# Performance work log

Measured on AMD Instinct MI355X. Metric: run time of the kernel, lower is better.

Reference implementation:

```python
import jax, jax.numpy as jnp
import numpy as np

B, P, ENC, DEC, ATT, EMB, V, MEM, TCAP = 64, 196, 2048, 512, 512, 512, 10000, 128, 22
T = TCAP - 1  # max decode length (caption_lengths - 1)


def setup_inputs() -> dict:
    key = jax.random.key(0)
    ks = iter(jax.random.split(key, 32))
    def w(shape, s=0.02):
        return (jax.random.normal(next(ks), shape, jnp.float32) * s)
    encoder_out = jax.random.normal(next(ks), (B, P, ENC), jnp.float32)
    encoded_captions = jax.random.randint(next(ks), (B, TCAP), 0, V)
    lens = np.sort(np.asarray(jax.random.randint(next(ks), (B,), 5, TCAP + 1)))[::-1].copy()
    lens[0] = TCAP  # ensure max(decode_lengths) == T
    caption_lengths = jnp.asarray(lens, jnp.int32)
    return {
        'encoder_out': encoder_out,
        'encoded_captions': encoded_captions,
        'caption_lengths': caption_lengths,
        'emb_table': w((V, EMB), 0.05),
        # Linear weights stored as [in, out] (torch W.T), so y = x @ W + b
        'W_enc': w((ENC, ATT)), 'b_enc': jnp.zeros((ATT,), jnp.float32),
        'W_dec': w((DEC, ATT)), 'b_dec': jnp.zeros((ATT,), jnp.float32),
        'W_full': w((ATT, 1)), 'b_full': jnp.zeros((1,), jnp.float32),
        'W_inith': w((ENC, DEC)), 'b_inith': jnp.zeros((DEC,), jnp.float32),
        'W_initc': w((ENC, DEC)), 'b_initc': jnp.zeros((DEC,), jnp.float32),
        'W_beta': w((DEC, ENC)), 'b_beta': jnp.zeros((ENC,), jnp.float32),
        # LSTMCell (torch gate order i, f, g, o), stored as [in, 4*dec]
        'W_ih': w((EMB + ENC, 4 * DEC)), 'b_ih': jnp.zeros((4 * DEC,), jnp.float32),
        'W_hh': w((DEC, 4 * DEC)), 'b_hh': jnp.zeros((4 * DEC,), jnp.float32),
        'memory_bank': jax.random.normal(next(ks), (MEM, DEC), jnp.float32),
        'W_fc': w((DEC, V)), 'b_fc': jnp.zeros((V,), jnp.float32),
    }


def _decode(encoder_out, encoded_captions, caption_lengths, emb_table,
            W_enc, b_enc, W_dec, b_dec, W_full, b_full,
            W_inith, b_inith, W_initc, b_initc, W_beta, b_beta,
            W_ih, b_ih, W_hh, b_hh, memory_bank, W_fc, b_fc):
    dec_len = caption_lengths - 1  # decode_lengths
    embs = emb_table[encoded_captions]                 # [B, TCAP, EMB]
    mean_enc = encoder_out.mean(axis=1)                # [B, ENC]
    h0 = mean_enc @ W_inith + b_inith
    c0 = mean_enc @ W_initc + b_initc
    att1 = encoder_out @ W_enc + b_enc                 # [B, P, ATT] precomputed

    x_seq = jnp.swapaxes(embs[:, :T, :], 0, 1)         # [T, B, EMB]
    mask_seq = jnp.arange(T)[:, None] < dec_len[None, :]  # [T, B]

    def step(carry, inp):
        h, c = carry
        x_t, m = inp                                   # [B,EMB], [B]
        # attention
        att2 = h @ W_dec + b_dec                       # [B, ATT]
        e = (jax.nn.relu(att1 + att2[:, None, :]) @ W_full)[..., 0] + b_full[0]  # [B, P]
        alpha = jax.nn.softmax(e, axis=1)
        awe = jnp.einsum('bpe,bp->be', encoder_out, alpha)  # [B, ENC]
        gate = jax.nn.sigmoid(h @ W_beta + b_beta)
        awe = gate * awe
        # LSTMCell
        xi = jnp.concatenate([x_t, awe], axis=1)
        gates = xi @ W_ih + b_ih + h @ W_hh + b_hh      # [B, 4*DEC]
        gi, gf, gg, go = jnp.split(gates, 4, axis=1)
        c_new = jax.nn.sigmoid(gf) * c + jax.nn.sigmoid(gi) * jnp.tanh(gg)
        h_new = jax.nn.sigmoid(go) * jnp.tanh(c_new)
        # hash memory
        sim = h_new @ memory_bank.T                    # [B, MEM]
        h_new = h_new + jax.nn.softmax(sim, axis=1) @ memory_bank
        # fc (dropout = identity in eval)
        preds = h_new @ W_fc + b_fc                    # [B, V]
        m2 = m[:, None]
        h = jnp.where(m2, h_new, h)
        c = jnp.where(m2, c_new, c)
        preds = jnp.where(m2, preds, 0.0)
        alpha = jnp.where(m2, alpha, 0.0)
        return (h, c), (preds, alpha)

    (_, _), (preds_seq, alpha_seq) = jax.lax.scan(step, (h0, c0), (x_seq, mask_seq))
    predictions = jnp.swapaxes(preds_seq, 0, 1)        # [B, T, V]
    alphas = jnp.swapaxes(alpha_seq, 0, 1)             # [B, T, P]
    return predictions, dec_len, alphas


def reference(encoder_out, encoded_captions, caption_lengths, emb_table,
              W_enc, b_enc, W_dec, b_dec, W_full, b_full,
              W_inith, b_inith, W_initc, b_initc, W_beta, b_beta,
              W_ih, b_ih, W_hh, b_hh, memory_bank, W_fc, b_fc):
    return _decode(encoder_out, encoded_captions, caption_lengths, emb_table,
                   W_enc, b_enc, W_dec, b_dec, W_full, b_full,
                   W_inith, b_inith, W_initc, b_initc, W_beta, b_beta,
                   W_ih, b_ih, W_hh, b_hh, memory_bank, W_fc, b_fc)
```

## Files before the change

### kernel.cpp

```cpp
#include <hip/hip_runtime.h>

#define BB   64
#define PP   196
#define ENCD 2048
#define DECD 512
#define VV   10000
#define TT   21
#define KIH  2560

typedef __attribute__((ext_vector_type(8))) short bf16x8;
typedef __attribute__((ext_vector_type(4))) float f32x4;

__device__ __forceinline__ float sigm(float x)   { return 1.f / (1.f + __expf(-x)); }
__device__ __forceinline__ float tanh_f(float x) { return 1.f - 2.f / (1.f + __expf(2.f * x)); }
__device__ __forceinline__ ushort f2bf(float x) {
    unsigned u = __float_as_uint(x);
    unsigned r = (u + 0x7FFFu + ((u >> 16) & 1u)) >> 16;
    return (ushort)r;
}
__device__ __forceinline__ float bf2f(short u) {
    return __uint_as_float(((unsigned)(ushort)u) << 16);
}
union U8 { float4 f4; ushort u[8]; };


__global__ void k_cvt(const float* __restrict__ in, ushort* __restrict__ out, int n4) {
    int i = blockIdx.x * 256 + threadIdx.x;
    if (i >= n4) return;
    float4 v = ((const float4*)in)[i];
    ushort4 o; o.x = f2bf(v.x); o.y = f2bf(v.y); o.z = f2bf(v.z); o.w = f2bf(v.w);
    ((ushort4*)out)[i] = o;
}

__global__ void k_mean16(const ushort* __restrict__ encB, float* __restrict__ mean) {
    int idx = blockIdx.x * 256 + threadIdx.x;
    int b = idx >> 10, e2 = idx & 1023;
    const uint* p = (const uint*)encB + (size_t)b * PP * 1024 + e2;
    float s0 = 0.f, s1 = 0.f;
    #pragma unroll 7
    for (int i = 0; i < PP; ++i) {
        uint v = p[(size_t)i * 1024];
        s0 += __uint_as_float(v << 16);
        s1 += __uint_as_float(v & 0xffff0000u);
    }
    mean[b * 2048 + e2 * 2]     = s0 * (1.f / 196.f);
    mean[b * 2048 + e2 * 2 + 1] = s1 * (1.f / 196.f);
}

__global__ __launch_bounds__(256) void k_ipart(const float* __restrict__ mean,
        const float* __restrict__ Wh, const float* __restrict__ Wc,
        float* __restrict__ ipart) {
    __shared__ alignas(16) float As[32][68];
    __shared__ alignas(16) float Bs[32][68];
    const int n0 = blockIdx.x * 64;
    const int kc = blockIdx.y;
    const int mat = blockIdx.z;
    const float* Bp = mat ? Wc : Wh;
    const int tid = threadIdx.x, tx = tid & 15, ty = tid >> 4;
    float acc[4][4] = {};
    for (int k0 = 0; k0 < 512; k0 += 32) {
        #pragma unroll
        for (int p = 0; p < 2; ++p) {
            int c = p * 256 + tid;
            int m = c >> 3, k4 = (c & 7) * 4;
            float4 v = *(const float4*)(mean + m * 2048 + kc * 512 + k0 + k4);
            As[k4 + 0][m] = v.x; As[k4 + 1][m] = v.y; As[k4 + 2][m] = v.z; As[k4 + 3][m] = v.w;
            int kb = c >> 4, n4 = (c & 15) * 4;
            float4 w = *(const float4*)(Bp + (size_t)(kc * 512 + k0 + kb) * 512 + n0 + n4);
            *(float4*)&Bs[kb][n4] = w;
        }
        __syncthreads();
        #pragma unroll 8
        for (int k = 0; k < 32; ++k) {
            float4 a = *(const float4*)&As[k][ty * 4];
            float4 b = *(const float4*)&Bs[k][tx * 4];
            float av[4] = {a.x, a.y, a.z, a.w}, bv[4] = {b.x, b.y, b.z, b.w};
            #pragma unroll
            for (int i = 0; i < 4; ++i)
                #pragma unroll
                for (int j = 0; j < 4; ++j) acc[i][j] += av[i] * bv[j];
        }
        __syncthreads();
    }
    #pragma unroll
    for (int i = 0; i < 4; ++i) {
        int m = ty * 4 + i;
        #pragma unroll
        for (int j = 0; j < 4; ++j) {
            int n = n0 + tx * 4 + j;
            ipart[((size_t)(mat * 4 + kc) * BB + m) * 512 + n] = acc[i][j];
        }
    }
}

__global__ void k_ifin(const float* __restrict__ ipart,
                       const float* __restrict__ bh, const float* __restrict__ bc,
                       float* __restrict__ h, float* __restrict__ c, ushort* __restrict__ hB) {
    int idx = blockIdx.x * 256 + threadIdx.x;
    int mat = idx >> 15, rem = idx & 32767;
    int b = rem >> 9, d = rem & 511;
    float s = 0.f;
    #pragma unroll
    for (int kc = 0; kc < 4; ++kc) s += ipart[((size_t)(mat * 4 + kc) * BB + b) * 512 + d];
    if (mat) c[rem] = s + bc[d];
    else { float v = s + bh[d]; h[rem] = v; hB[rem] = f2bf(v); }
}

__global__ __launch_bounds__(256) void k_tcvt_all(
        const float* __restrict__ Wenc, const float* __restrict__ Wdec,
        const float* __restrict__ Wbeta, const float* __restrict__ Whh,
        const float* __restrict__ Wih, const float* __restrict__ Wfc,
        ushort* __restrict__ WencT, ushort* __restrict__ WdecT,
        ushort* __restrict__ WbetaT, ushort* __restrict__ WhhT,
        ushort* __restrict__ WihT, ushort* __restrict__ WfcT) {
    __shared__ float lds[64 * 65];
    int l = blockIdx.x;
    const float* in; ushort* out; int K, N, KT;
    if (l < 256)       { in = Wenc;  out = WencT;  K = 2048; N = 512;   KT = 32; }
    else if (l < 320)  { l -= 256;  in = Wdec;  out = WdecT;  K = 512;  N = 512;   KT = 8; }
    else if (l < 576)  { l -= 320;  in = Wbeta; out = WbetaT; K = 512;  N = 2048;  KT = 8; }
    else if (l < 832)  { l -= 576;  in = Whh;   out = WhhT;   K = 512;  N = 2048;  KT = 8; }
    else if (l < 2112) { l -= 832;  in = Wih;   out = WihT;   K = KIH;  N = 2048;  KT = 40; }
    else               { l -= 2112; in = Wfc;   out = WfcT;   K = 512;  N = 10000; KT = 8; }
    const int k0 = (l % KT) * 64, n0 = (l / KT) * 64;
    const int tid = threadIdx.x;
    for (int i = tid; i < 4096; i += 256) {
        int kk = i >> 6, nn = i & 63;
        float v = 0.f;
        if (n0 + nn < N) v = in[(size_t)(k0 + kk) * N + n0 + nn];
        lds[nn * 65 + kk] = v;
    }
    __syncthreads();
    for (int i = tid; i < 4096; i += 256) {
        int nn = i >> 6, kk = i & 63;
        out[(size_t)(n0 + nn) * K + k0 + kk] = f2bf(lds[nn * 65 + kk]);
    }
}

__global__ __launch_bounds__(256) void k_att1_256(const ushort* __restrict__ A,
        const ushort* __restrict__ Bt, const float* __restrict__ bias,
        ushort* __restrict__ C) {
    __shared__ alignas(16) ushort As[64 * 64];
    __shared__ alignas(16) ushort Bs[256 * 64];
    const int n0 = blockIdx.x * 256;
    const int m0 = blockIdx.y * 64;
    const int tid = threadIdx.x, wid = tid >> 6, lane = tid & 63;
    f32x4 acc[4][4] = {};
    for (int k0 = 0; k0 < 2048; k0 += 64) {
        #pragma unroll
        for (int p = 0; p < 2; ++p) {
            int c = p * 256 + tid;
            int r = c >> 3, cc = c & 7;
            float4 v = *(const float4*)(A + (size_t)(m0 + r) * 2048 + k0 + cc * 8);
            *(float4*)(As + r * 64 + ((cc ^ (r & 7)) * 8)) = v;
        }
        #pragma unroll
        for (int p = 0; p < 8; ++p) {
            int c = p * 256 + tid;
            int r = c >> 3, cc = c & 7;
            float4 v = *(const float4*)(Bt + (size_t)(n0 + r) * 2048 + k0 + cc * 8);
            *(float4*)(Bs + r * 64 + ((cc ^ (r & 7)) * 8)) = v;
        }
        __syncthreads();
        #pragma unroll
        for (int kk = 0; kk < 2; ++kk) {
            int ci = kk * 4 + (lane >> 4);
            bf16x8 afrag[4], bfrag[4];
            #pragma unroll
            for (int m = 0; m < 4; ++m) {
                int row = m * 16 + (lane & 15);
                afrag[m] = *(const bf16x8*)(As + row * 64 + ((ci ^ (row & 7)) * 8));
            }
            #pragma unroll
            for (int n = 0; n < 4; ++n) {
                int col = wid * 64 + n * 16 + (lane & 15);
                bfrag[n] = *(const bf16x8*)(Bs + col * 64 + ((ci ^ (col & 7)) * 8));
            }
            #pragma unroll
            for (int m = 0; m < 4; ++m)
                #pragma unroll
                for (int n = 0; n < 4; ++n)
                    acc[m][n] = __builtin_amdgcn_mfma_f32_16x16x32_bf16(afrag[m], bfrag[n], acc[m][n], 0, 0, 0);
        }
        __syncthreads();
    }
    #pragma unroll
    for (int m = 0; m < 4; ++m) {
        int rb = m0 + m * 16 + (lane >> 4) * 4;
        #pragma unroll
        for (int n = 0; n < 4; ++n) {
            int col = n0 + wid * 64 + n * 16 + (lane & 15);
            float bv = bias[col];
            #pragma unroll
            for (int r = 0; r < 4; ++r)
                C[(size_t)(rb + r) * 512 + col] = f2bf(acc[m][n][r] + bv);
        }
    }
}

__global__ void k_declen(const int* __restrict__ lens, float* __restrict__ out) {
    int b = threadIdx.x;
    if (b < BB) out[b] = (float)(lens[b] - 1);
}


__global__ __launch_bounds__(256) void k_hgemm64(const ushort* __restrict__ hB,
        const float* __restrict__ emb, const int* __restrict__ caps, int t,
        const ushort* __restrict__ WdecT, const float* __restrict__ bd,
        const ushort* __restrict__ WbetaT, const float* __restrict__ bb,
        const ushort* __restrict__ WhhT, const ushort* __restrict__ WihT,
        float* __restrict__ att2, float* __restrict__ gate, float* __restrict__ hhp) {
    __shared__ alignas(16) ushort As[64 * 64];
    __shared__ alignas(16) ushort Bs[64 * 64];
    __shared__ int capsh[64];
    const int bx = blockIdx.x;
    int seg, n0;
    if (bx < 8)       { seg = 0; n0 = bx * 64; }
    else if (bx < 40) { seg = 1; n0 = (bx - 8) * 64; }
    else              { seg = 2; n0 = (bx - 40) * 64; }
    const int tid = threadIdx.x, wid = tid >> 6, lane = tid & 63;
    if (tid < 64) capsh[tid] = caps[tid * 22 + t];
    __syncthreads();
    const int KSEG = (seg == 2) ? 1024 : 512;
    f32x4 acc[4] = {};
    for (int k0 = 0; k0 < KSEG; k0 += 64) {
        const bool second = k0 >= 512;
        #pragma unroll
        for (int p = 0; p < 2; ++p) {
            int c = p * 256 + tid;
            int r = c >> 3, cc = c & 7;
            if (!second) {
                float4 v = *(const float4*)(hB + r * 512 + k0 + cc * 8);
                *(float4*)(As + r * 64 + ((cc ^ (r & 7)) * 8)) = v;
            } else {
                const float* er = emb + (size_t)capsh[r] * 512 + (k0 - 512) + cc * 8;
                float4 v0 = *(const float4*)er;
                float4 v1 = *(const float4*)(er + 4);
                U8 pk;
                pk.u[0] = f2bf(v0.x); pk.u[1] = f2bf(v0.y); pk.u[2] = f2bf(v0.z); pk.u[3] = f2bf(v0.w);
                pk.u[4] = f2bf(v1.x); pk.u[5] = f2bf(v1.y); pk.u[6] = f2bf(v1.z); pk.u[7] = f2bf(v1.w);
                *(float4*)(As + r * 64 + ((cc ^ (r & 7)) * 8)) = pk.f4;
            }
            const ushort* brow;
            if (seg == 0)      brow = WdecT + (size_t)(n0 + r) * 512 + k0 + cc * 8;
            else if (seg == 1) brow = WbetaT + (size_t)(n0 + r) * 512 + k0 + cc * 8;
            else brow = second ? (WihT + (size_t)(n0 + r) * KIH + (k0 - 512) + cc * 8)
                               : (WhhT + (size_t)(n0 + r) * 512 + k0 + cc * 8);
            float4 v = *(const float4*)brow;
            *(float4*)(Bs + r * 64 + ((cc ^ (r & 7)) * 8)) = v;
        }
        __syncthreads();
        #pragma unroll
        for (int kk = 0; kk < 2; ++kk) {
            int ci = kk * 4 + (lane >> 4);
            int colL = wid * 16 + (lane & 15);
            bf16x8 bfrag = *(const bf16x8*)(Bs + colL * 64 + ((ci ^ (colL & 7)) * 8));
            #pragma unroll
            for (int m = 0; m < 4; ++m) {
                int row = m * 16 + (lane & 15);
                bf16x8 afrag = *(const bf16x8*)(As + row * 64 + ((ci ^ (row & 7)) * 8));
                acc[m] = __builtin_amdgcn_mfma_f32_16x16x32_bf16(afrag, bfrag, acc[m], 0, 0, 0);
            }
        }
        __syncthreads();
    }
    int colL = wid * 16 + (lane & 15);
    int col = n0 + colL;
    #pragma unroll
    for (int m = 0; m < 4; ++m) {
        int rb = m * 16 + (lane >> 4) * 4;
        #pragma unroll
        for (int r = 0; r < 4; ++r) {
            int row = rb + r;
            float v = acc[m][r];
            if (seg == 0)      att2[row * 512 + col] = v + bd[col];
            else if (seg == 1) gate[row * 2048 + col] = sigm(v + bb[col]);
            else               hhp[(size_t)row * 2048 + col] = v;
        }
    }
}

__global__ __launch_bounds__(256) void k_escore_p(const ushort* __restrict__ att1B,
        const float* __restrict__ att2, const float* __restrict__ Wf,
        float* __restrict__ es) {
    __shared__ float a2[512], wf[512];
    int b = blockIdx.y, pc = blockIdx.x, tid = threadIdx.x;
    for (int i = tid; i < 512; i += 256) { a2[i] = att2[b * 512 + i]; wf[i] = Wf[i]; }
    __syncthreads();
    int lane = tid & 63, wid = tid >> 6;
    for (int i = wid; i < 49; i += 4) {
        int p = pc * 49 + i;
        bf16x8 rv = *(const bf16x8*)(att1B + ((size_t)(b * PP + p)) * 512 + lane * 8);
        float s = 0.f;
        #pragma unroll
        for (int j = 0; j < 8; ++j) {
            float v = bf2f(rv[j]) + a2[lane * 8 + j];
            s += (v > 0.f ? v : 0.f) * wf[lane * 8 + j];
        }
        #pragma unroll
        for (int off = 32; off; off >>= 1) s += __shfl_down(s, off);
        if (lane == 0) es[b * 256 + p] = s;
    }
}

__global__ __launch_bounds__(256) void k_awe16s(const ushort* __restrict__ encB,
        const float* __restrict__ es, const float* __restrict__ gate,
        const int* __restrict__ lens, int t,
        uint* __restrict__ aweB, float* __restrict__ out_alpha) {
    __shared__ float al[224], red[256];
    int b = blockIdx.y, pc = blockIdx.x, tid = threadIdx.x;
    float v = (tid < PP) ? es[b * 256 + tid] : -3.4e38f;
    red[tid] = v; __syncthreads();
    for (int s = 128; s; s >>= 1) { if (tid < s) red[tid] = fmaxf(red[tid], red[tid + s]); __syncthreads(); }
    float mx = red[0]; __syncthreads();
    float ev = (tid < PP) ? __expf(v - mx) : 0.f;
    red[tid] = ev; __syncthreads();
    for (int s = 128; s; s >>= 1) { if (tid < s) red[tid] += red[tid + s]; __syncthreads(); }
    float inv = 1.f / red[0];
    if (tid < PP) {
        float a = ev * inv;
        al[tid] = a;
        if (pc == 0) {
            bool m = t < (lens[b] - 1);
            out_alpha[((size_t)b * TT + t) * PP + tid] = m ? a : 0.f;
        }
    }
    __syncthreads();
    int pair = pc * 128 + (tid >> 1);
    int half = tid & 1;
    const uint* p = (const uint*)encB + (size_t)b * PP * 1024 + pair;
    float s0 = 0.f, s1 = 0.f;
    int i0 = half * 98;
    #pragma unroll 7
    for (int i = i0; i < i0 + 98; ++i) {
        uint vv = p[(size_t)i * 1024];
        float a = al[i];
        s0 += a * __uint_as_float(vv << 16);
        s1 += a * __uint_as_float(vv & 0xffff0000u);
    }
    s0 += __shfl_xor(s0, 1);
    s1 += __shfl_xor(s1, 1);
    if (half == 0) {
        int e = pair * 2;
        float g0 = s0 * gate[b * 2048 + e];
        float g1 = s1 * gate[b * 2048 + e + 1];
        aweB[b * 1024 + pair] = (uint)f2bf(g0) | ((uint)f2bf(g1) << 16);
    }
}

__global__ __launch_bounds__(256) void k_gawe64(const ushort* __restrict__ aweB,
        const ushort* __restrict__ WihT, float* __restrict__ pawe) {
    __shared__ alignas(16) ushort As[64 * 64];
    __shared__ alignas(16) ushort Bs[64 * 64];
    const int n0 = blockIdx.x * 64;
    const int kc = blockIdx.y;
    const int tid = threadIdx.x, wid = tid >> 6, lane = tid & 63;
    f32x4 acc[4] = {};
    for (int k0 = 0; k0 < 512; k0 += 64) {
        #pragma unroll
        for (int p = 0; p < 2; ++p) {
            int c = p * 256 + tid;
            int r = c >> 3, cc = c & 7;
            float4 v = *(const float4*)(aweB + r * 2048 + kc * 512 + k0 + cc * 8);
            *(float4*)(As + r * 64 + ((cc ^ (r & 7)) * 8)) = v;
            float4 w = *(const float4*)(WihT + (size_t)(n0 + r) * KIH + 512 + kc * 512 + k0 + cc * 8);
            *(float4*)(Bs + r * 64 + ((cc ^ (r & 7)) * 8)) = w;
        }
        __syncthreads();
        #pragma unroll
        for (int kk = 0; kk < 2; ++kk) {
            int ci = kk * 4 + (lane >> 4);
            int colL = wid * 16 + (lane & 15);
            bf16x8 bfrag = *(const bf16x8*)(Bs + colL * 64 + ((ci ^ (colL & 7)) * 8));
            #pragma unroll
            for (int m = 0; m < 4; ++m) {
                int row = m * 16 + (lane & 15);
                bf16x8 afrag = *(const bf16x8*)(As + row * 64 + ((ci ^ (row & 7)) * 8));
                acc[m] = __builtin_amdgcn_mfma_f32_16x16x32_bf16(afrag, bfrag, acc[m], 0, 0, 0);
            }
        }
        __syncthreads();
    }
    int col = n0 + wid * 16 + (lane & 15);
    #pragma unroll
    for (int m = 0; m < 4; ++m) {
        int rb = m * 16 + (lane >> 4) * 4;
        #pragma unroll
        for (int r = 0; r < 4; ++r)
            pawe[((size_t)kc * BB + rb + r) * 2048 + col] = acc[m][r];
    }
}

__global__ __launch_bounds__(256) void k_memattn(const float* __restrict__ hhp,
        const float* __restrict__ pawe,
        const float* __restrict__ bih, const float* __restrict__ bhh,
        const int* __restrict__ lens, int t, const float* __restrict__ memB,
        float* __restrict__ h, float* __restrict__ c,
        ushort* __restrict__ hB, ushort* __restrict__ histB) {
    __shared__ float hs[512], sims[128], red[256], ps[128];
    int b = blockIdx.x, tid = threadIdx.x;
    bool msk = t < (lens[b] - 1);
    for (int j = tid; j < 512; j += 256) {
        float g[4];
        #pragma unroll
        for (int q = 0; q < 4; ++q) {
            int col = q * 512 + j;
            float s = bih[col] + bhh[col] + hhp[(size_t)b * 2048 + col];
            #pragma unroll
            for (int kc = 0; kc < 4; ++kc) s += pawe[((size_t)kc * BB + b) * 2048 + col];
            g[q] = s;
        }
        float gi = sigm(g[0]), gf = sigm(g[1]), gg = tanh_f(g[2]), go = sigm(g[3]);
        float cold = c[b * 512 + j];
        float cn = gf * cold + gi * gg;
        c[b * 512 + j] = msk ? cn : cold;
        hs[j] = go * tanh_f(cn);
    }
    __syncthreads();
    int lane = tid & 63, wid = tid >> 6;
    for (int m = wid * 32; m < wid * 32 + 32; ++m) {
        const float* r = memB + (size_t)m * 512 + lane * 8;
        float4 r0 = *(const float4*)(r);
        float4 r1 = *(const float4*)(r + 4);
        float4 h0 = *(const float4*)(&hs[lane * 8]);
        float4 h1 = *(const float4*)(&hs[lane * 8 + 4]);
        float s = r0.x * h0.x + r0.y * h0.y + r0.z * h0.z + r0.w * h0.w
                + r1.x * h1.x + r1.y * h1.y + r1.z * h1.z + r1.w * h1.w;
        #pragma unroll
        for (int off = 32; off; off >>= 1) s += __shfl_down(s, off);
        if (lane == 0) sims[m] = s;
    }
    __syncthreads();
    float v = (tid < 128) ? sims[tid] : -3.4e38f;
    red[tid] = v; __syncthreads();
    for (int s = 128; s; s >>= 1) { if (tid < s) red[tid] = fmaxf(red[tid], red[tid + s]); __syncthreads(); }
    float mx = red[0]; __syncthreads();
    float ev = (tid < 128) ? __expf(v - mx) : 0.f;
    red[tid] = ev; __syncthreads();
    for (int s = 128; s; s >>= 1) { if (tid < s) red[tid] += red[tid + s]; __syncthreads(); }
    if (tid < 128) ps[tid] = ev / red[0];
    __syncthreads();
    for (int d = tid; d < 512; d += 256) {
        float s = 0.f;
        #pragma unroll 4
        for (int m = 0; m < 128; ++m) s += ps[m] * memB[(size_t)m * 512 + d];
        float hn = hs[d] + s;
        histB[((size_t)t * BB + b) * 512 + d] = f2bf(hn);
        float hold = h[b * 512 + d];
        float hv = msk ? hn : hold;
        h[b * 512 + d] = hv;
        hB[b * 512 + d] = f2bf(hv);
    }
}

__global__ __launch_bounds__(256) void k_preds_batch(const ushort* __restrict__ histB,
        const ushort* __restrict__ WfcT, const float* __restrict__ bfc,
        const int* __restrict__ lens, float* __restrict__ out) {
    __shared__ alignas(16) ushort As[64 * 64];
    __shared__ alignas(16) ushort Bs[256 * 64];
    const int n0 = blockIdx.x * 256;
    const int t = blockIdx.y;
    const ushort* A = histB + (size_t)t * BB * 512;
    const int tid = threadIdx.x, wid = tid >> 6, lane = tid & 63;
    f32x4 acc[4][4] = {};
    for (int k0 = 0; k0 < 512; k0 += 64) {
        #pragma unroll
        for (int p = 0; p < 2; ++p) {
            int c = p * 256 + tid;
            int r = c >> 3, cc = c & 7;
            float4 v = *(const float4*)(A + r * 512 + k0 + cc * 8);
            *(float4*)(As + r * 64 + ((cc ^ (r & 7)) * 8)) = v;
        }
        #pragma unroll
        for (int p = 0; p < 8; ++p) {
            int c = p * 256 + tid;
            int r = c >> 3, cc = c & 7;
            float4 v = *(const float4*)(WfcT + (size_t)(n0 + r) * 512 + k0 + cc * 8);
            *(float4*)(Bs + r * 64 + ((cc ^ (r & 7)) * 8)) = v;
        }
        __syncthreads();
        #pragma unroll
        for (int kk = 0; kk < 2; ++kk) {
            int ci = kk * 4 + (lane >> 4);
            bf16x8 afrag[4], bfrag[4];
            #pragma unroll
            for (int m = 0; m < 4; ++m) {
                int row = m * 16 + (lane & 15);
                afrag[m] = *(const bf16x8*)(As + row * 64 + ((ci ^ (row & 7)) * 8));
            }
            #pragma unroll
            for (int n = 0; n < 4; ++n) {
                int col = wid * 64 + n * 16 + (lane & 15);
                bfrag[n] = *(const bf16x8*)(Bs + col * 64 + ((ci ^ (col & 7)) * 8));
            }
            #pragma unroll
            for (int m = 0; m < 4; ++m)
                #pragma unroll
                for (int n = 0; n < 4; ++n)
                    acc[m][n] = __builtin_amdgcn_mfma_f32_16x16x32_bf16(afrag[m], bfrag[n], acc[m][n], 0, 0, 0);
        }
        __syncthreads();
    }
    #pragma unroll
    for (int m = 0; m < 4; ++m) {
        int rb = m * 16 + (lane >> 4) * 4;
        #pragma unroll
        for (int n = 0; n < 4; ++n) {
            int col = n0 + wid * 64 + n * 16 + (lane & 15);
            if (col < VV) {
                float bv = bfc[col];
                #pragma unroll
                for (int r = 0; r < 4; ++r) {
                    int b = rb + r;
                    bool msk = t < (lens[b] - 1);
                    out[((size_t)b * TT + t) * VV + col] = msk ? (acc[m][n][r] + bv) : 0.f;
                }
            }
        }
    }
}


extern "C" void kernel_launch(void* const* d_in, const int* in_sizes, int n_in,
                              void* d_out, int out_size, void* d_ws, size_t ws_size,
                              hipStream_t stream) {
    const float* enc     = (const float*)d_in[0];
    const int*   caps    = (const int*)d_in[1];
    const int*   lens    = (const int*)d_in[2];
    const float* emb     = (const float*)d_in[3];
    const float* W_enc   = (const float*)d_in[4];
    const float* b_enc   = (const float*)d_in[5];
    const float* W_dec   = (const float*)d_in[6];
    const float* b_dec   = (const float*)d_in[7];
    const float* W_full  = (const float*)d_in[8];
    const float* W_inith = (const float*)d_in[10];
    const float* b_inith = (const float*)d_in[11];
    const float* W_initc = (const float*)d_in[12];
    const float* b_initc = (const float*)d_in[13];
    const float* W_beta  = (const float*)d_in[14];
    const float* b_beta  = (const float*)d_in[15];
    const float* W_ih    = (const float*)d_in[16];
    const float* b_ih    = (const float*)d_in[17];
    const float* W_hh    = (const float*)d_in[18];
    const float* b_hh    = (const float*)d_in[19];
    const float* memB    = (const float*)d_in[20];
    const float* W_fc    = (const float*)d_in[21];
    const float* b_fc    = (const float*)d_in[22];

    float* out = (float*)d_out;
    float* preds_out  = out;
    float* declen_out = out + (size_t)BB * TT * VV;
    float* alpha_out  = declen_out + BB;

    float* ws    = (float*)d_ws;
    ushort* att1B = (ushort*)ws;        ws += (size_t)12544 * 512 / 2;
    float* h     = ws;  ws += BB * DECD;
    float* c     = ws;  ws += BB * DECD;
    float* att2  = ws;  ws += BB * 512;
    float* gate  = ws;  ws += BB * ENCD;
    float* es    = ws;  ws += BB * 256;
    float* hhp   = ws;  ws += BB * 2048;
    float* pawe  = ws;  ws += (size_t)4 * BB * 2048;
    ushort* hB   = (ushort*)ws;  ws += BB * DECD / 2;
    uint*  aweB  = (uint*)ws;    ws += BB * ENCD / 2;
    ushort* histB = (ushort*)ws; ws += (size_t)TT * BB * DECD / 2;
    ushort* encB  = (ushort*)ws; ws += (size_t)12544 * 2048 / 2;
    ushort* WencT = (ushort*)ws; ws += (size_t)512 * 2048 / 2;
    ushort* WfcT  = (ushort*)ws; ws += (size_t)10240 * 512 / 2;
    ushort* WdecT = (ushort*)ws; ws += (size_t)512 * 512 / 2;
    ushort* WbetaT= (ushort*)ws; ws += (size_t)2048 * 512 / 2;
    ushort* WhhT  = (ushort*)ws; ws += (size_t)2048 * 512 / 2;
    ushort* WihT  = (ushort*)ws; ws += (size_t)2048 * KIH / 2;
    float* ipart = hhp;
    float* mean  = (float*)att1B;

    k_cvt<<<(12544 * 2048 / 4 + 255) / 256, 256, 0, stream>>>(enc, encB, 12544 * 2048 / 4);
    k_mean16<<<256, 256, 0, stream>>>(encB, mean);
    k_ipart<<<dim3(8, 4, 2), 256, 0, stream>>>(mean, W_inith, W_initc, ipart);
    k_ifin<<<256, 256, 0, stream>>>(ipart, b_inith, b_initc, h, c, hB);
    k_declen<<<1, 64, 0, stream>>>(lens, declen_out);
    k_tcvt_all<<<3392, 256, 0, stream>>>(W_enc, W_dec, W_beta, W_hh, W_ih, W_fc,
                                         WencT, WdecT, WbetaT, WhhT, WihT, WfcT);
    k_att1_256<<<dim3(2, 196), 256, 0, stream>>>(encB, WencT, b_enc, att1B);

    for (int t = 0; t < TT; ++t) {
        k_hgemm64<<<72, 256, 0, stream>>>(hB, emb, caps, t, WdecT, b_dec, WbetaT, b_beta,
                                          WhhT, WihT, att2, gate, hhp);
        k_escore_p<<<dim3(4, 64), 256, 0, stream>>>(att1B, att2, W_full, es);
        k_awe16s<<<dim3(8, 64), 256, 0, stream>>>(encB, es, gate, lens, t, aweB, alpha_out);
        k_gawe64<<<dim3(32, 4), 256, 0, stream>>>((const ushort*)aweB, WihT, pawe);
        k_memattn<<<64, 256, 0, stream>>>(hhp, pawe, b_ih, b_hh, lens, t, memB, h, c, hB, histB);
    }
    k_preds_batch<<<dim3(40, TT), 256, 0, stream>>>(histB, WfcT, b_fc, lens, preds_out);
}
```

Before: 1.965 ms.

## Precompute embedding input projection for all timesteps and merge recurrent weights

The embedding half of the LSTM input GEMM does not depend on the recurrence, so it is hoisted out of the time loop into one batched GEMM over all timesteps (k_xpre) whose result is read in the gate kernel. The per-step hidden GEMM now uses a single concatenated transposed weight (Wdec|Wbeta|Whh) with uniform K=512, which removes the longer K=1024 segment and the branchy per-segment loads. The attention-weighted encoding kernel is re-split to 16 column chunks with 4 waves striding over pixels plus an LDS reduction. The cost is extra workspace for the per-step precomputed projections.

```diff
diff --git a/kernel.cpp b/kernel.cpp
--- a/kernel.cpp
+++ b/kernel.cpp
@@ -18,8 +18,8 @@
     unsigned r = (u + 0x7FFFu + ((u >> 16) & 1u)) >> 16;
     return (ushort)r;
 }
-__device__ __forceinline__ float bf2f(short u) {
-    return __uint_as_float(((unsigned)(ushort)u) << 16);
+__device__ __forceinline__ float bf2f(ushort u) {
+    return __uint_as_float(((unsigned)u) << 16);
 }
 union U8 { float4 f4; ushort u[8]; };
 
@@ -137,7 +137,7 @@
     }
 }
 
-__global__ __launch_bounds__(256) void k_att1_256(const ushort* __restrict__ A,
+__global__ __launch_bounds__(256) void k_att1n(const ushort* __restrict__ A,
         const ushort* __restrict__ Bt, const float* __restrict__ bias,
         ushort* __restrict__ C) {
     __shared__ alignas(16) ushort As[64 * 64];
@@ -198,56 +198,98 @@
     }
 }
 
+__global__ __launch_bounds__(256) void k_xpre(const float* __restrict__ emb,
+        const int* __restrict__ caps, const ushort* __restrict__ WihT,
+        float* __restrict__ xpre) {
+    __shared__ alignas(16) ushort As[64 * 64];
+    __shared__ alignas(16) ushort Bs[256 * 64];
+    __shared__ int capsh[64];
+    const int n0 = blockIdx.x * 256;
+    const int t = blockIdx.y;
+    const int tid = threadIdx.x, wid = tid >> 6, lane = tid & 63;
+    if (tid < 64) capsh[tid] = caps[tid * 22 + t];
+    __syncthreads();
+    f32x4 acc[4][4] = {};
+    for (int k0 = 0; k0 < 512; k0 += 64) {
+        #pragma unroll
+        for (int p = 0; p < 2; ++p) {
+            int c = p * 256 + tid;
+            int r = c >> 3, cc = c & 7;
+            const float* er = emb + (size_t)capsh[r] * 512 + k0 + cc * 8;
+            float4 v0 = *(const float4*)er;
+            float4 v1 = *(const float4*)(er + 4);
+            U8 pk;
+            pk.u[0] = f2bf(v0.x); pk.u[1] = f2bf(v0.y); pk.u[2] = f2bf(v0.z); pk.u[3] = f2bf(v0.w);
+            pk.u[4] = f2bf(v1.x); pk.u[5] = f2bf(v1.y); pk.u[6] = f2bf(v1.z); pk.u[7] = f2bf(v1.w);
+            *(float4*)(As + r * 64 + ((cc ^ (r & 7)) * 8)) = pk.f4;
+        }
+        #pragma unroll
+        for (int p = 0; p < 8; ++p) {
+            int c = p * 256 + tid;
+            int r = c >> 3, cc = c & 7;
+            float4 v = *(const float4*)(WihT + (size_t)(n0 + r) * KIH + k0 + cc * 8);
+            *(float4*)(Bs + r * 64 + ((cc ^ (r & 7)) * 8)) = v;
+        }
+        __syncthreads();
+        #pragma unroll
+        for (int kk = 0; kk < 2; ++kk) {
+            int ci = kk * 4 + (lane >> 4);
+            bf16x8 afrag[4], bfrag[4];
+            #pragma unroll
+            for (int m = 0; m < 4; ++m) {
+                int row = m * 16 + (lane & 15);
+                afrag[m] = *(const bf16x8*)(As + row * 64 + ((ci ^ (row & 7)) * 8));
+            }
+            #pragma unroll
+            for (int n = 0; n < 4; ++n) {
+                int col = wid * 64 + n * 16 + (lane & 15);
+                bfrag[n] = *(const bf16x8*)(Bs + col * 64 + ((ci ^ (col & 7)) * 8));
+            }
+            #pragma unroll
+            for (int m = 0; m < 4; ++m)
+                #pragma unroll
+                for (int n = 0; n < 4; ++n)
+                    acc[m][n] = __builtin_amdgcn_mfma_f32_16x16x32_bf16(afrag[m], bfrag[n], acc[m][n], 0, 0, 0);
+        }
+        __syncthreads();
+    }
+    #pragma unroll
+    for (int m = 0; m < 4; ++m) {
+        int rb = m * 16 + (lane >> 4) * 4;
+        #pragma unroll
+        for (int n = 0; n < 4; ++n) {
+            int col = n0 + wid * 64 + n * 16 + (lane & 15);
+            #pragma unroll
+            for (int r = 0; r < 4; ++r)
+                xpre[((size_t)t * BB + rb + r) * 2048 + col] = acc[m][n][r];
+        }
+    }
+}
+
 __global__ void k_declen(const int* __restrict__ lens, float* __restrict__ out) {
     int b = threadIdx.x;
     if (b < BB) out[b] = (float)(lens[b] - 1);
 }
 
 
-__global__ __launch_bounds__(256) void k_hgemm64(const ushort* __restrict__ hB,
-        const float* __restrict__ emb, const int* __restrict__ caps, int t,
-        const ushort* __restrict__ WdecT, const float* __restrict__ bd,
-        const ushort* __restrict__ WbetaT, const float* __restrict__ bb,
-        const ushort* __restrict__ WhhT, const ushort* __restrict__ WihT,
-        float* __restrict__ att2, float* __restrict__ gate, float* __restrict__ hhp) {
+__global__ __launch_bounds__(256) void k_p1(const ushort* __restrict__ hB,
+        const ushort* __restrict__ WcatT, const float* __restrict__ bd,
+        const float* __restrict__ bb, float* __restrict__ att2,
+        float* __restrict__ gate, float* __restrict__ hhp) {
     __shared__ alignas(16) ushort As[64 * 64];
     __shared__ alignas(16) ushort Bs[64 * 64];
-    __shared__ int capsh[64];
-    const int bx = blockIdx.x;
-    int seg, n0;
-    if (bx < 8)       { seg = 0; n0 = bx * 64; }
-    else if (bx < 40) { seg = 1; n0 = (bx - 8) * 64; }
-    else              { seg = 2; n0 = (bx - 40) * 64; }
-    const int tid = threadIdx.x, wid = tid >> 6, lane = tid & 63;
-    if (tid < 64) capsh[tid] = caps[tid * 22 + t];
-    __syncthreads();
-    const int KSEG = (seg == 2) ? 1024 : 512;
+    const int tid = threadIdx.x, lane = tid & 63, wid = tid >> 6;
+    const int n0 = blockIdx.x * 64;
     f32x4 acc[4] = {};
-    for (int k0 = 0; k0 < KSEG; k0 += 64) {
-        const bool second = k0 >= 512;
+    for (int k0 = 0; k0 < 512; k0 += 64) {
         #pragma unroll
         for (int p = 0; p < 2; ++p) {
-            int c = p * 256 + tid;
-            int r = c >> 3, cc = c & 7;
-            if (!second) {
-                float4 v = *(const float4*)(hB + r * 512 + k0 + cc * 8);
-                *(float4*)(As + r * 64 + ((cc ^ (r & 7)) * 8)) = v;
-            } else {
-                const float* er = emb + (size_t)capsh[r] * 512 + (k0 - 512) + cc * 8;
-                float4 v0 = *(const float4*)er;
-                float4 v1 = *(const float4*)(er + 4);
-                U8 pk;
-                pk.u[0] = f2bf(v0.x); pk.u[1] = f2bf(v0.y); pk.u[2] = f2bf(v0.z); pk.u[3] = f2bf(v0.w);
-                pk.u[4] = f2bf(v1.x); pk.u[5] = f2bf(v1.y); pk.u[6] = f2bf(v1.z); pk.u[7] = f2bf(v1.w);
-                *(float4*)(As + r * 64 + ((cc ^ (r & 7)) * 8)) = pk.f4;
-            }
-            const ushort* brow;
-            if (seg == 0)      brow = WdecT + (size_t)(n0 + r) * 512 + k0 + cc * 8;
-            else if (seg == 1) brow = WbetaT + (size_t)(n0 + r) * 512 + k0 + cc * 8;
-            else brow = second ? (WihT + (size_t)(n0 + r) * KIH + (k0 - 512) + cc * 8)
-                               : (WhhT + (size_t)(n0 + r) * 512 + k0 + cc * 8);
-            float4 v = *(const float4*)brow;
-            *(float4*)(Bs + r * 64 + ((cc ^ (r & 7)) * 8)) = v;
+            int c8 = p * 256 + tid;
+            int r = c8 >> 3, cc = c8 & 7;
+            float4 v = *(const float4*)(hB + r * 512 + k0 + cc * 8);
+            *(float4*)(As + r * 64 + ((cc ^ (r & 7)) * 8)) = v;
+            float4 w = *(const float4*)(WcatT + (size_t)(n0 + r) * 512 + k0 + cc * 8);
+            *(float4*)(Bs + r * 64 + ((cc ^ (r & 7)) * 8)) = w;
         }
         __syncthreads();
         #pragma unroll
@@ -264,8 +306,7 @@
         }
         __syncthreads();
     }
-    int colL = wid * 16 + (lane & 15);
-    int col = n0 + colL;
+    int col = n0 + wid * 16 + (lane & 15);
     #pragma unroll
     for (int m = 0; m < 4; ++m) {
         int rb = m * 16 + (lane >> 4) * 4;
@@ -273,9 +314,9 @@
         for (int r = 0; r < 4; ++r) {
             int row = rb + r;
             float v = acc[m][r];
-            if (seg == 0)      att2[row * 512 + col] = v + bd[col];
-            else if (seg == 1) gate[row * 2048 + col] = sigm(v + bb[col]);
-            else               hhp[(size_t)row * 2048 + col] = v;
+            if (col < 512)       att2[row * 512 + col] = v + bd[col];
+            else if (col < 2560) gate[row * 2048 + (col - 512)] = sigm(v + bb[col - 512]);
+            else                 hhp[(size_t)row * 2048 + (col - 2560)] = v;
         }
     }
 }
@@ -294,7 +335,7 @@
         float s = 0.f;
         #pragma unroll
         for (int j = 0; j < 8; ++j) {
-            float v = bf2f(rv[j]) + a2[lane * 8 + j];
+            float v = bf2f((ushort)rv[j]) + a2[lane * 8 + j];
             s += (v > 0.f ? v : 0.f) * wf[lane * 8 + j];
         }
         #pragma unroll
@@ -306,9 +347,9 @@
 __global__ __launch_bounds__(256) void k_awe16s(const ushort* __restrict__ encB,
         const float* __restrict__ es, const float* __restrict__ gate,
         const int* __restrict__ lens, int t,
-        uint* __restrict__ aweB, float* __restrict__ out_alpha) {
-    __shared__ float al[224], red[256];
-    int b = blockIdx.y, pc = blockIdx.x, tid = threadIdx.x;
+        uint* __restrict__ aweB, float* __restrict__ alpha_out) {
+    __shared__ float al[224], red[256], ps0[4][64], ps1[4][64];
+    int b = blockIdx.y, ec = blockIdx.x, tid = threadIdx.x;
     float v = (tid < PP) ? es[b * 256 + tid] : -3.4e38f;
     red[tid] = v; __syncthreads();
     for (int s = 128; s; s >>= 1) { if (tid < s) red[tid] = fmaxf(red[tid], red[tid + s]); __syncthreads(); }
@@ -320,48 +361,50 @@
     if (tid < PP) {
         float a = ev * inv;
         al[tid] = a;
-        if (pc == 0) {
+        if (ec == 0) {
             bool m = t < (lens[b] - 1);
-            out_alpha[((size_t)b * TT + t) * PP + tid] = m ? a : 0.f;
-        }
-    }
-    __syncthreads();
-    int pair = pc * 128 + (tid >> 1);
-    int half = tid & 1;
-    const uint* p = (const uint*)encB + (size_t)b * PP * 1024 + pair;
+            alpha_out[((size_t)b * TT + t) * PP + tid] = m ? a : 0.f;
+        }
+    }
+    __syncthreads();
+    int w = tid >> 6, lane = tid & 63;
+    int pair = ec * 64 + lane;
+    const uint* pp = (const uint*)encB + (size_t)b * PP * 1024 + pair;
     float s0 = 0.f, s1 = 0.f;
-    int i0 = half * 98;
     #pragma unroll 7
-    for (int i = i0; i < i0 + 98; ++i) {
-        uint vv = p[(size_t)i * 1024];
+    for (int i = w; i < PP; i += 4) {
+        uint vv = pp[(size_t)i * 1024];
         float a = al[i];
         s0 += a * __uint_as_float(vv << 16);
         s1 += a * __uint_as_float(vv & 0xffff0000u);
     }
-    s0 += __shfl_xor(s0, 1);
-    s1 += __shfl_xor(s1, 1);
-    if (half == 0) {
-        int e = pair * 2;
-        float g0 = s0 * gate[b * 2048 + e];
-        float g1 = s1 * gate[b * 2048 + e + 1];
-        aweB[b * 1024 + pair] = (uint)f2bf(g0) | ((uint)f2bf(g1) << 16);
-    }
-}
-
-__global__ __launch_bounds__(256) void k_gawe64(const ushort* __restrict__ aweB,
+    ps0[w][lane] = s0; ps1[w][lane] = s1;
+    __syncthreads();
+    if (tid < 64) {
+        float t0 = ps0[0][tid] + ps0[1][tid] + ps0[2][tid] + ps0[3][tid];
+        float t1 = ps1[0][tid] + ps1[1][tid] + ps1[2][tid] + ps1[3][tid];
+        int e = (ec * 64 + tid) * 2;
+        float g0 = t0 * gate[b * 2048 + e];
+        float g1 = t1 * gate[b * 2048 + e + 1];
+        ushort u0 = f2bf(g0), u1 = f2bf(g1);
+        aweB[b * 1024 + ec * 64 + tid] = (uint)u0 | ((uint)u1 << 16);
+    }
+}
+
+__global__ __launch_bounds__(256) void k_p3(const uint* __restrict__ aweB,
         const ushort* __restrict__ WihT, float* __restrict__ pawe) {
     __shared__ alignas(16) ushort As[64 * 64];
     __shared__ alignas(16) ushort Bs[64 * 64];
-    const int n0 = blockIdx.x * 64;
-    const int kc = blockIdx.y;
-    const int tid = threadIdx.x, wid = tid >> 6, lane = tid & 63;
+    const int tid = threadIdx.x, lane = tid & 63, wid = tid >> 6;
+    const int n0 = (blockIdx.x & 31) * 64, kc = blockIdx.x >> 5;
+    const ushort* aweU = (const ushort*)aweB;
     f32x4 acc[4] = {};
     for (int k0 = 0; k0 < 512; k0 += 64) {
         #pragma unroll
         for (int p = 0; p < 2; ++p) {
-            int c = p * 256 + tid;
-            int r = c >> 3, cc = c & 7;
-            float4 v = *(const float4*)(aweB + r * 2048 + kc * 512 + k0 + cc * 8);
+            int c8 = p * 256 + tid;
+            int r = c8 >> 3, cc = c8 & 7;
+            float4 v = *(const float4*)(aweU + r * 2048 + kc * 512 + k0 + cc * 8);
             *(float4*)(As + r * 64 + ((cc ^ (r & 7)) * 8)) = v;
             float4 w = *(const float4*)(WihT + (size_t)(n0 + r) * KIH + 512 + kc * 512 + k0 + cc * 8);
             *(float4*)(Bs + r * 64 + ((cc ^ (r & 7)) * 8)) = w;
@@ -391,21 +434,24 @@
     }
 }
 
-__global__ __launch_bounds__(256) void k_memattn(const float* __restrict__ hhp,
-        const float* __restrict__ pawe,
+__global__ __launch_bounds__(256) void k_p4(const float* __restrict__ hhp,
+        const float* __restrict__ pawe, const float* __restrict__ xpre,
         const float* __restrict__ bih, const float* __restrict__ bhh,
         const int* __restrict__ lens, int t, const float* __restrict__ memB,
         float* __restrict__ h, float* __restrict__ c,
         ushort* __restrict__ hB, ushort* __restrict__ histB) {
-    __shared__ float hs[512], sims[128], red[256], ps[128];
-    int b = blockIdx.x, tid = threadIdx.x;
+    __shared__ float hss[512], simss[128], reds[256], pss[128];
+    const int b = blockIdx.x, tid = threadIdx.x;
+    const int lane = tid & 63, wid = tid >> 6;
     bool msk = t < (lens[b] - 1);
     for (int j = tid; j < 512; j += 256) {
         float g[4];
         #pragma unroll
         for (int q = 0; q < 4; ++q) {
             int col = q * 512 + j;
-            float s = bih[col] + bhh[col] + hhp[(size_t)b * 2048 + col];
+            float s = bih[col] + bhh[col]
+                    + hhp[(size_t)b * 2048 + col]
+                    + xpre[((size_t)t * BB + b) * 2048 + col];
             #pragma unroll
             for (int kc = 0; kc < 4; ++kc) s += pawe[((size_t)kc * BB + b) * 2048 + col];
             g[q] = s;
@@ -414,37 +460,36 @@
         float cold = c[b * 512 + j];
         float cn = gf * cold + gi * gg;
         c[b * 512 + j] = msk ? cn : cold;
-        hs[j] = go * tanh_f(cn);
-    }
-    __syncthreads();
-    int lane = tid & 63, wid = tid >> 6;
+        hss[j] = go * tanh_f(cn);
+    }
+    __syncthreads();
     for (int m = wid * 32; m < wid * 32 + 32; ++m) {
         const float* r = memB + (size_t)m * 512 + lane * 8;
         float4 r0 = *(const float4*)(r);
         float4 r1 = *(const float4*)(r + 4);
-        float4 h0 = *(const float4*)(&hs[lane * 8]);
-        float4 h1 = *(const float4*)(&hs[lane * 8 + 4]);
+        float4 h0 = *(const float4*)(&hss[lane * 8]);
+        float4 h1 = *(const float4*)(&hss[lane * 8 + 4]);
         float s = r0.x * h0.x + r0.y * h0.y + r0.z * h0.z + r0.w * h0.w
                 + r1.x * h1.x + r1.y * h1.y + r1.z * h1.z + r1.w * h1.w;
         #pragma unroll
         for (int off = 32; off; off >>= 1) s += __shfl_down(s, off);
-        if (lane == 0) sims[m] = s;
-    }
-    __syncthreads();
-    float v = (tid < 128) ? sims[tid] : -3.4e38f;
-    red[tid] = v; __syncthreads();
-    for (int s = 128; s; s >>= 1) { if (tid < s) red[tid] = fmaxf(red[tid], red[tid + s]); __syncthreads(); }
-    float mx = red[0]; __syncthreads();
+        if (lane == 0) simss[m] = s;
+    }
+    __syncthreads();
+    float v = (tid < 128) ? simss[tid] : -3.4e38f;
+    reds[tid] = v; __syncthreads();
+    for (int s = 128; s; s >>= 1) { if (tid < s) reds[tid] = fmaxf(reds[tid], reds[tid + s]); __syncthreads(); }
+    float mx = reds[0]; __syncthreads();
     float ev = (tid < 128) ? __expf(v - mx) : 0.f;
-    red[tid] = ev; __syncthreads();
-    for (int s = 128; s; s >>= 1) { if (tid < s) red[tid] += red[tid + s]; __syncthreads(); }
-    if (tid < 128) ps[tid] = ev / red[0];
+    reds[tid] = ev; __syncthreads();
+    for (int s = 128; s; s >>= 1) { if (tid < s) reds[tid] += reds[tid + s]; __syncthreads(); }
+    if (tid < 128) pss[tid] = ev / reds[0];
     __syncthreads();
     for (int d = tid; d < 512; d += 256) {
         float s = 0.f;
         #pragma unroll 4
-        for (int m = 0; m < 128; ++m) s += ps[m] * memB[(size_t)m * 512 + d];
-        float hn = hs[d] + s;
+        for (int m = 0; m < 128; ++m) s += pss[m] * memB[(size_t)m * 512 + d];
+        float hn = hss[d] + s;
         histB[((size_t)t * BB + b) * 512 + d] = f2bf(hn);
         float hold = h[b * 512 + d];
         float hv = msk ? hn : hold;
@@ -553,26 +598,25 @@
     float* alpha_out  = declen_out + BB;
 
     float* ws    = (float*)d_ws;
-    ushort* att1B = (ushort*)ws;        ws += (size_t)12544 * 512 / 2;
+    ushort* att1B = (ushort*)ws;  ws += (size_t)12544 * 512 / 2;
     float* h     = ws;  ws += BB * DECD;
     float* c     = ws;  ws += BB * DECD;
     float* att2  = ws;  ws += BB * 512;
-    float* gate  = ws;  ws += BB * ENCD;
+    float* gate  = ws;  ws += BB * 2048;
+    float* hhp   = ws;  ws += BB * 2048;
     float* es    = ws;  ws += BB * 256;
-    float* hhp   = ws;  ws += BB * 2048;
     float* pawe  = ws;  ws += (size_t)4 * BB * 2048;
+    float* xpre  = ws;  ws += (size_t)TT * BB * 2048;
     ushort* hB   = (ushort*)ws;  ws += BB * DECD / 2;
-    uint*  aweB  = (uint*)ws;    ws += BB * ENCD / 2;
+    uint*  aweB  = (uint*)ws;    ws += BB * 1024;
     ushort* histB = (ushort*)ws; ws += (size_t)TT * BB * DECD / 2;
     ushort* encB  = (ushort*)ws; ws += (size_t)12544 * 2048 / 2;
     ushort* WencT = (ushort*)ws; ws += (size_t)512 * 2048 / 2;
     ushort* WfcT  = (ushort*)ws; ws += (size_t)10240 * 512 / 2;
-    ushort* WdecT = (ushort*)ws; ws += (size_t)512 * 512 / 2;
-    ushort* WbetaT= (ushort*)ws; ws += (size_t)2048 * 512 / 2;
-    ushort* WhhT  = (ushort*)ws; ws += (size_t)2048 * 512 / 2;
+    ushort* WcatT = (ushort*)ws; ws += (size_t)4608 * 512 / 2;
     ushort* WihT  = (ushort*)ws; ws += (size_t)2048 * KIH / 2;
-    float* ipart = hhp;
     float* mean  = (float*)att1B;
+    float* ipart = xpre;
 
     k_cvt<<<(12544 * 2048 / 4 + 255) / 256, 256, 0, stream>>>(enc, encB, 12544 * 2048 / 4);
     k_mean16<<<256, 256, 0, stream>>>(encB, mean);
@@ -580,16 +624,18 @@
     k_ifin<<<256, 256, 0, stream>>>(ipart, b_inith, b_initc, h, c, hB);
     k_declen<<<1, 64, 0, stream>>>(lens, declen_out);
     k_tcvt_all<<<3392, 256, 0, stream>>>(W_enc, W_dec, W_beta, W_hh, W_ih, W_fc,
-                                         WencT, WdecT, WbetaT, WhhT, WihT, WfcT);
-    k_att1_256<<<dim3(2, 196), 256, 0, stream>>>(encB, WencT, b_enc, att1B);
+                                         WencT, WcatT, WcatT + (size_t)512 * 512,
+                                         WcatT + (size_t)2560 * 512, WihT, WfcT);
+    k_att1n<<<dim3(2, 196), 256, 0, stream>>>(encB, WencT, b_enc, att1B);
+    k_xpre<<<dim3(8, TT), 256, 0, stream>>>(emb, caps, WihT, xpre);
 
     for (int t = 0; t < TT; ++t) {
-        k_hgemm64<<<72, 256, 0, stream>>>(hB, emb, caps, t, WdecT, b_dec, WbetaT, b_beta,
-                                          WhhT, WihT, att2, gate, hhp);
+        k_p1<<<72, 256, 0, stream>>>(hB, WcatT, b_dec, b_beta, att2, gate, hhp);
         k_escore_p<<<dim3(4, 64), 256, 0, stream>>>(att1B, att2, W_full, es);
-        k_awe16s<<<dim3(8, 64), 256, 0, stream>>>(encB, es, gate, lens, t, aweB, alpha_out);
-        k_gawe64<<<dim3(32, 4), 256, 0, stream>>>((const ushort*)aweB, WihT, pawe);
-        k_memattn<<<64, 256, 0, stream>>>(hhp, pawe, b_ih, b_hh, lens, t, memB, h, c, hB, histB);
-    }
+        k_awe16s<<<dim3(16, 64), 256, 0, stream>>>(encB, es, gate, lens, t, aweB, alpha_out);
+        k_p3<<<128, 256, 0, stream>>>(aweB, WihT, pawe);
+        k_p4<<<64, 256, 0, stream>>>(hhp, pawe, xpre, b_ih, b_hh, lens, t, memB, h, c, hB, histB);
+    }
+
     k_preds_batch<<<dim3(40, TT), 256, 0, stream>>>(histB, WfcT, b_fc, lens, preds_out);
 }
```

Measured after the change: 1.687 ms. 14.1% less time.
